# Optimization experiments

Hardware: AMD Instinct MI355X
Metric: run time of the kernel (lower is better)

Reference implementation:

```python
import jax, jax.numpy as jnp
import numpy as np

N, E = 50000, 800000
IN_DIM, HID, OUT_DIM = 512, 64, 40


def setup_inputs() -> dict:
    key = jax.random.key(0)
    ks = jax.random.split(key, 7)
    X = jax.random.normal(ks[0], (N, IN_DIM), dtype=jnp.float32)
    edges = jax.random.randint(ks[1], (2, E), 0, N, dtype=jnp.int64)
    # GCNConv weight (glorot) and bias
    W1 = jax.random.normal(ks[2], (IN_DIM, HID), dtype=jnp.float32) / np.sqrt(IN_DIM)
    b1 = jnp.zeros((HID,), dtype=jnp.float32)
    # fc Linear
    Wfc = jax.random.normal(ks[3], (OUT_DIM, HID), dtype=jnp.float32) / np.sqrt(HID)
    bfc = jax.random.normal(ks[4], (OUT_DIM,), dtype=jnp.float32) * 0.01
    return {"X": X, "edges": edges, "W1": W1, "b1": b1, "Wfc": Wfc, "bfc": bfc}


def gcn_conv(x, src, dst, W, b, n):
    # PyG GCNConv: transform, add self-loops, symmetric D^-1/2 A D^-1/2 norm,
    # scatter-add messages at destination, add bias.
    h = x @ W  # [N, HID]
    loop = jnp.arange(n, dtype=src.dtype)
    src = jnp.concatenate([src, loop])
    dst = jnp.concatenate([dst, loop])
    deg = jax.ops.segment_sum(jnp.ones_like(dst, dtype=h.dtype), dst, num_segments=n)
    dinv = jnp.where(deg > 0, jax.lax.rsqrt(deg), 0.0)
    coef = dinv[src] * dinv[dst]  # [E+N]
    msgs = coef[:, None] * h[src]  # gather + scale
    agg = jax.ops.segment_sum(msgs, dst, num_segments=n)  # scatter-add
    return agg + b


def reference(X, edges, W1, b1, Wfc, bfc):
    n = X.shape[0]
    src, dst = edges[0], edges[1]
    h = jax.nn.relu(gcn_conv(X, src, dst, W1, b1, n))  # [N, HID]
    return h @ Wfc.T + bfc  # [N, OUT_DIM]
```

## Files before the change

kernel.cpp:

```cpp
#include <hip/hip_runtime.h>
#include <hip/hip_bf16.h>

typedef unsigned short u16;
typedef __bf16 bf16_8 __attribute__((ext_vector_type(8)));
typedef float f32_4 __attribute__((ext_vector_type(4)));

#define IN_DIM 512
#define HID 64
#define OUT_DIM 40
#define CAP 64
#define CF_BLOCKS 512

__global__ void k_prep(const float* __restrict__ W1, u16* __restrict__ W1t,
                       int* __restrict__ cnt, int n) {
    int i = blockIdx.x * 256 + threadIdx.x;
    if (i < n) cnt[i] = 0;
    if (i < IN_DIM * HID) {
        int k = i / HID, o = i % HID;
        __hip_bfloat16 v = __float2bfloat16(W1[i]);
        W1t[o * IN_DIM + k] = *reinterpret_cast<u16*>(&v);
    }
}

__launch_bounds__(256)
__global__ void k_work(const float* __restrict__ X, const u16* __restrict__ W1t,
                       const int* __restrict__ src, const int* __restrict__ dst,
                       int* cnt, u16* __restrict__ csr, u16* __restrict__ hs,
                       int N, int E, int NT) {
    __shared__ __align__(16) u16 As[2][64 * 40];
    const int t = threadIdx.x;

    if ((int)blockIdx.x >= NT) {
        const int slice = (int)blockIdx.x & 7;
        const int rank  = ((int)blockIdx.x - NT) >> 3;
        const int lo = (int)(((long)slice * N) >> 3);
        const int hi = (int)(((long)(slice + 1) * N) >> 3);
        const int stride = 64 * 256;
        int e = rank * 256 + t;
        for (; e + 3 * stride < E; e += 4 * stride) {
            int d0 = dst[e];
            int d1 = dst[e + stride];
            int d2 = dst[e + 2 * stride];
            int d3 = dst[e + 3 * stride];
            if (d0 >= lo && d0 < hi) {
                int p = atomicAdd(&cnt[d0], 1);
                if (p < CAP) csr[(size_t)d0 * CAP + p] = (u16)src[e];
            }
            if (d1 >= lo && d1 < hi) {
                int p = atomicAdd(&cnt[d1], 1);
                if (p < CAP) csr[(size_t)d1 * CAP + p] = (u16)src[e + stride];
            }
            if (d2 >= lo && d2 < hi) {
                int p = atomicAdd(&cnt[d2], 1);
                if (p < CAP) csr[(size_t)d2 * CAP + p] = (u16)src[e + 2 * stride];
            }
            if (d3 >= lo && d3 < hi) {
                int p = atomicAdd(&cnt[d3], 1);
                if (p < CAP) csr[(size_t)d3 * CAP + p] = (u16)src[e + 3 * stride];
            }
        }
        for (; e < E; e += stride) {
            int d = dst[e];
            if (d >= lo && d < hi) {
                int p = atomicAdd(&cnt[d], 1);
                if (p < CAP) csr[(size_t)d * CAP + p] = (u16)src[e];
            }
        }
        return;
    }

    const int wave = t >> 6;
    const int lane = t & 63;
    const int m = lane & 15;
    const int quad = lane >> 4;
    const int n0 = blockIdx.x * 64;

    f32_4 acc[4];
    #pragma unroll
    for (int c = 0; c < 4; c++) acc[c] = (f32_4){0.f, 0.f, 0.f, 0.f};

    const int r_st = t >> 2;
    const int k_st = (t & 3) * 8;

    int row = n0 + r_st; if (row >= N) row = N - 1;
    const float* xp = X + (size_t)row * IN_DIM + k_st;

    f32_4 x0 = *reinterpret_cast<const f32_4*>(xp);
    f32_4 x1 = *reinterpret_cast<const f32_4*>(xp + 4);

    int buf = 0;
    for (int k0 = 0; k0 < IN_DIM; k0 += 32) {
        u16 xb[8];
        #pragma unroll
        for (int q = 0; q < 4; q++) {
            __hip_bfloat16 c0 = __float2bfloat16(x0[q]);
            __hip_bfloat16 c1 = __float2bfloat16(x1[q]);
            xb[q]     = *reinterpret_cast<u16*>(&c0);
            xb[4 + q] = *reinterpret_cast<u16*>(&c1);
        }
        *reinterpret_cast<uint4*>(&As[buf][r_st * 40 + k_st]) = *reinterpret_cast<uint4*>(xb);
        __syncthreads();

        if (k0 + 32 < IN_DIM) {
            x0 = *reinterpret_cast<const f32_4*>(xp + k0 + 32);
            x1 = *reinterpret_cast<const f32_4*>(xp + k0 + 36);
        }

        bf16_8 a = *reinterpret_cast<const bf16_8*>(&As[buf][(wave * 16 + m) * 40 + quad * 8]);
        #pragma unroll
        for (int c = 0; c < 4; c++) {
            bf16_8 b = *reinterpret_cast<const bf16_8*>(
                W1t + (size_t)(c * 16 + m) * IN_DIM + k0 + quad * 8);
            acc[c] = __builtin_amdgcn_mfma_f32_16x16x32_bf16(a, b, acc[c], 0, 0, 0);
        }
        buf ^= 1;
    }

    const int nbase = n0 + wave * 16 + quad * 4;
    #pragma unroll
    for (int r = 0; r < 4; r++) {
        int n = nbase + r;
        if (n < N) {
            #pragma unroll
            for (int c = 0; c < 4; c++) {
                __hip_bfloat16 hv = __float2bfloat16(acc[c][r]);
                hs[(size_t)n * HID + c * 16 + m] = *reinterpret_cast<u16*>(&hv);
            }
        }
    }
}

__global__ void k_scale(u16* __restrict__ hs, const int* __restrict__ cnt, int N) {
    int i = blockIdx.x * 256 + threadIdx.x;
    int node = i >> 3;
    if (node >= N) return;
    float dv = rsqrtf((float)cnt[node] + 1.0f);
    uint4 v = *reinterpret_cast<uint4*>(hs + (size_t)i * 8);
    uint vv[4] = {v.x, v.y, v.z, v.w};
    u16 o[8];
    #pragma unroll
    for (int q = 0; q < 4; q++) {
        float lo = __uint_as_float(vv[q] << 16) * dv;
        float hi = __uint_as_float(vv[q] & 0xFFFF0000u) * dv;
        __hip_bfloat16 bl_ = __float2bfloat16(lo);
        __hip_bfloat16 bh_ = __float2bfloat16(hi);
        o[2 * q]     = *reinterpret_cast<u16*>(&bl_);
        o[2 * q + 1] = *reinterpret_cast<u16*>(&bh_);
    }
    *reinterpret_cast<uint4*>(hs + (size_t)i * 8) = *reinterpret_cast<uint4*>(o);
}

__device__ __forceinline__ void acc_add(f32_4& a, uint2 v) {
    a[0] += __uint_as_float(v.x << 16);
    a[1] += __uint_as_float(v.x & 0xFFFF0000u);
    a[2] += __uint_as_float(v.y << 16);
    a[3] += __uint_as_float(v.y & 0xFFFF0000u);
}

#define SHP 72

__launch_bounds__(256)
__global__ void k_aggfc(const u16* __restrict__ hs, const u16* __restrict__ csr,
                        const int* __restrict__ cnt, const float* __restrict__ b1,
                        const float* __restrict__ Wfc, const float* __restrict__ bfc,
                        float* __restrict__ out, int N) {
    __shared__ __align__(16) u16 shb[16 * SHP];
    __shared__ __align__(16) u16 wfb[48 * SHP];
    __shared__ float bl[48];
    const int t = threadIdx.x;

    for (int i = t; i < 48 * HID; i += 256) {
        int o = i / HID, k = i % HID;
        float v = (o < OUT_DIM) ? Wfc[o * HID + k] : 0.f;
        __hip_bfloat16 b = __float2bfloat16(v);
        wfb[o * SHP + k] = *reinterpret_cast<u16*>(&b);
    }
    if (t < 48) bl[t] = (t < OUT_DIM) ? bfc[t] : 0.f;

    const int g = t >> 4, l = t & 15;
    const int n = blockIdx.x * 16 + g;

    if (n < N) {
        const uint2* hs2 = reinterpret_cast<const uint2*>(hs);
        f32_4 aa[4];
        #pragma unroll
        for (int q = 0; q < 4; q++) aa[q] = (f32_4){0.f, 0.f, 0.f, 0.f};
        const float dvn = rsqrtf((float)cnt[n] + 1.0f);
        acc_add(aa[0], hs2[(size_t)n * 16 + l]);
        int deg = cnt[n]; if (deg > CAP) deg = CAP;
        uint2 cv = reinterpret_cast<const uint2*>(csr + (size_t)n * CAP)[l];
        const int nn1 = N - 1;
        for (int j = 0; j < deg; j += 16) {
            int base = j >> 2;
            uint wx[4], wy[4];
            #pragma unroll
            for (int q = 0; q < 4; q++) {
                wx[q] = __shfl(cv.x, base + q, 16);
                wy[q] = __shfl(cv.y, base + q, 16);
            }
            int s[16];
            #pragma unroll
            for (int q = 0; q < 4; q++) {
                s[4 * q + 0] = (int)(wx[q] & 0xffff);
                s[4 * q + 1] = (int)(wx[q] >> 16);
                s[4 * q + 2] = (int)(wy[q] & 0xffff);
                s[4 * q + 3] = (int)(wy[q] >> 16);
            }
            uint2 v[16];
            #pragma unroll
            for (int i = 0; i < 16; i++) {
                int si = s[i] < nn1 ? s[i] : nn1;
                v[i] = hs2[(size_t)si * 16 + l];
            }
            #pragma unroll
            for (int i = 0; i < 16; i++) {
                if (j + i >= deg) { v[i].x = 0u; v[i].y = 0u; }
                acc_add(aa[i & 3], v[i]);
            }
        }
        f32_4 acc = (aa[0] + aa[1]) + (aa[2] + aa[3]);
        u16 rb[4];
        #pragma unroll
        for (int q = 0; q < 4; q++) {
            float x = dvn * acc[q] + b1[l * 4 + q];
            x = x > 0.f ? x : 0.f;
            __hip_bfloat16 hb = __float2bfloat16(x);
            rb[q] = *reinterpret_cast<u16*>(&hb);
        }
        *reinterpret_cast<uint2*>(&shb[g * SHP + l * 4]) = *reinterpret_cast<uint2*>(rb);
    }
    __syncthreads();

    const int wave = t >> 6;
    const int lane = t & 63;
    const int m = lane & 15;
    const int quad = lane >> 4;
    if (wave < 3) {
        bf16_8 a0 = *reinterpret_cast<const bf16_8*>(&shb[m * SHP + quad * 8]);
        bf16_8 a1 = *reinterpret_cast<const bf16_8*>(&shb[m * SHP + 32 + quad * 8]);
        bf16_8 b0 = *reinterpret_cast<const bf16_8*>(&wfb[(wave * 16 + m) * SHP + quad * 8]);
        bf16_8 b1 = *reinterpret_cast<const bf16_8*>(&wfb[(wave * 16 + m) * SHP + 32 + quad * 8]);
        f32_4 c = (f32_4){0.f, 0.f, 0.f, 0.f};
        c = __builtin_amdgcn_mfma_f32_16x16x32_bf16(a0, b0, c, 0, 0, 0);
        c = __builtin_amdgcn_mfma_f32_16x16x32_bf16(a1, b1, c, 0, 0, 0);
        const int o = wave * 16 + m;
        if (o < OUT_DIM) {
            const int base = blockIdx.x * 16;
            #pragma unroll
            for (int r = 0; r < 4; r++) {
                int node = base + quad * 4 + r;
                if (node < N) out[(size_t)node * OUT_DIM + o] = c[r] + bl[o];
            }
        }
    }
}


extern "C" void kernel_launch(void* const* d_in, const int* in_sizes, int n_in,
                              void* d_out, int out_size, void* d_ws, size_t ws_size,
                              hipStream_t stream) {
    const float* X   = (const float*)d_in[0];
    const int* edges = (const int*)d_in[1];
    const float* W1  = (const float*)d_in[2];
    const float* b1  = (const float*)d_in[3];
    const float* Wfc = (const float*)d_in[4];
    const float* bfc = (const float*)d_in[5];

    const int N = in_sizes[0] / IN_DIM;
    const int E = in_sizes[1] / 2;
    const int* src = edges;
    const int* dst = edges + E;

    char* p = (char*)d_ws;
    auto carve = [&](size_t bytes) -> char* {
        char* r = p;
        p += (bytes + 255) & ~(size_t)255;
        return r;
    };
    u16* W1t = (u16*)carve((size_t)IN_DIM * HID * 2);
    u16* hs  = (u16*)carve((size_t)N * HID * 2);
    int* cnt = (int*)carve((size_t)N * 4);
    u16* csr = (u16*)carve((size_t)N * CAP * 2);

    const int nb = (N + 255) / 256;
    const int NT = (N + 63) / 64;

    k_prep <<<nb, 256, 0, stream>>>(W1, W1t, cnt, N);
    k_work <<<NT + CF_BLOCKS, 256, 0, stream>>>(X, W1t, src, dst, cnt, csr, hs, N, E, NT);
    k_scale<<<(N * 8 + 255) / 256, 256, 0, stream>>>(hs, cnt, N);
    k_aggfc<<<(N + 15) / 16, 256, 0, stream>>>(hs, csr, cnt, b1, Wfc, bfc,
                                               (float*)d_out, N);
}
```

Measured before the change: 249.4 us.

## Widen GEMM K-step to 64 and simplify CSR fill to unpartitioned atomics

The GEMM part of k_work now handles 64 K-elements per iteration, with a wider padded LDS tile, two MFMAs per output column block and an extra barrier per iteration. This halves the number of loop iterations and barriers and raises in-flight global loads per thread. Separately, the CSR-building blocks no longer split destinations into 8 slices with a 4-way unrolled scan. Each edge is now processed once with a grid-stride loop, which removes the redundant dst reads across slices but loses the locality of atomics grouped by slice.

```diff
diff --git a/kernel.cpp b/kernel.cpp
--- a/kernel.cpp
+++ b/kernel.cpp
@@ -27,44 +27,16 @@
                        const int* __restrict__ src, const int* __restrict__ dst,
                        int* cnt, u16* __restrict__ csr, u16* __restrict__ hs,
                        int N, int E, int NT) {
-    __shared__ __align__(16) u16 As[2][64 * 40];
+    __shared__ __align__(16) u16 As[2][64 * 72];
     const int t = threadIdx.x;
 
     if ((int)blockIdx.x >= NT) {
-        const int slice = (int)blockIdx.x & 7;
-        const int rank  = ((int)blockIdx.x - NT) >> 3;
-        const int lo = (int)(((long)slice * N) >> 3);
-        const int hi = (int)(((long)(slice + 1) * N) >> 3);
-        const int stride = 64 * 256;
-        int e = rank * 256 + t;
-        for (; e + 3 * stride < E; e += 4 * stride) {
-            int d0 = dst[e];
-            int d1 = dst[e + stride];
-            int d2 = dst[e + 2 * stride];
-            int d3 = dst[e + 3 * stride];
-            if (d0 >= lo && d0 < hi) {
-                int p = atomicAdd(&cnt[d0], 1);
-                if (p < CAP) csr[(size_t)d0 * CAP + p] = (u16)src[e];
-            }
-            if (d1 >= lo && d1 < hi) {
-                int p = atomicAdd(&cnt[d1], 1);
-                if (p < CAP) csr[(size_t)d1 * CAP + p] = (u16)src[e + stride];
-            }
-            if (d2 >= lo && d2 < hi) {
-                int p = atomicAdd(&cnt[d2], 1);
-                if (p < CAP) csr[(size_t)d2 * CAP + p] = (u16)src[e + 2 * stride];
-            }
-            if (d3 >= lo && d3 < hi) {
-                int p = atomicAdd(&cnt[d3], 1);
-                if (p < CAP) csr[(size_t)d3 * CAP + p] = (u16)src[e + 3 * stride];
-            }
-        }
-        for (; e < E; e += stride) {
+        int tid = ((int)blockIdx.x - NT) * 256 + t;
+        int stride = CF_BLOCKS * 256;
+        for (int e = tid; e < E; e += stride) {
             int d = dst[e];
-            if (d >= lo && d < hi) {
-                int p = atomicAdd(&cnt[d], 1);
-                if (p < CAP) csr[(size_t)d * CAP + p] = (u16)src[e];
-            }
+            int p = atomicAdd(&cnt[d], 1);
+            if (p < CAP) csr[(size_t)d * CAP + p] = (u16)src[e];
         }
         return;
     }
@@ -80,39 +52,54 @@
     for (int c = 0; c < 4; c++) acc[c] = (f32_4){0.f, 0.f, 0.f, 0.f};
 
     const int r_st = t >> 2;
-    const int k_st = (t & 3) * 8;
+    const int c2 = t & 3;
 
     int row = n0 + r_st; if (row >= N) row = N - 1;
-    const float* xp = X + (size_t)row * IN_DIM + k_st;
+    const float* xp = X + (size_t)row * IN_DIM + c2 * 16;
 
     f32_4 x0 = *reinterpret_cast<const f32_4*>(xp);
     f32_4 x1 = *reinterpret_cast<const f32_4*>(xp + 4);
+    f32_4 x2 = *reinterpret_cast<const f32_4*>(xp + 8);
+    f32_4 x3 = *reinterpret_cast<const f32_4*>(xp + 12);
 
     int buf = 0;
-    for (int k0 = 0; k0 < IN_DIM; k0 += 32) {
-        u16 xb[8];
+    for (int k0 = 0; k0 < IN_DIM; k0 += 64) {
+        u16 xb[16];
         #pragma unroll
         for (int q = 0; q < 4; q++) {
             __hip_bfloat16 c0 = __float2bfloat16(x0[q]);
             __hip_bfloat16 c1 = __float2bfloat16(x1[q]);
-            xb[q]     = *reinterpret_cast<u16*>(&c0);
-            xb[4 + q] = *reinterpret_cast<u16*>(&c1);
-        }
-        *reinterpret_cast<uint4*>(&As[buf][r_st * 40 + k_st]) = *reinterpret_cast<uint4*>(xb);
+            __hip_bfloat16 c2_ = __float2bfloat16(x2[q]);
+            __hip_bfloat16 c3 = __float2bfloat16(x3[q]);
+            xb[q]      = *reinterpret_cast<u16*>(&c0);
+            xb[4 + q]  = *reinterpret_cast<u16*>(&c1);
+            xb[8 + q]  = *reinterpret_cast<u16*>(&c2_);
+            xb[12 + q] = *reinterpret_cast<u16*>(&c3);
+        }
+        u16* wp = &As[buf][r_st * 72 + c2 * 16];
+        *reinterpret_cast<uint4*>(wp)     = *reinterpret_cast<uint4*>(&xb[0]);
+        *reinterpret_cast<uint4*>(wp + 8) = *reinterpret_cast<uint4*>(&xb[8]);
         __syncthreads();
 
-        if (k0 + 32 < IN_DIM) {
-            x0 = *reinterpret_cast<const f32_4*>(xp + k0 + 32);
-            x1 = *reinterpret_cast<const f32_4*>(xp + k0 + 36);
-        }
-
-        bf16_8 a = *reinterpret_cast<const bf16_8*>(&As[buf][(wave * 16 + m) * 40 + quad * 8]);
+        if (k0 + 64 < IN_DIM) {
+            x0 = *reinterpret_cast<const f32_4*>(xp + k0 + 64);
+            x1 = *reinterpret_cast<const f32_4*>(xp + k0 + 68);
+            x2 = *reinterpret_cast<const f32_4*>(xp + k0 + 72);
+            x3 = *reinterpret_cast<const f32_4*>(xp + k0 + 76);
+        }
+
+        bf16_8 a0 = *reinterpret_cast<const bf16_8*>(&As[buf][(wave * 16 + m) * 72 + quad * 8]);
+        bf16_8 a1 = *reinterpret_cast<const bf16_8*>(&As[buf][(wave * 16 + m) * 72 + 32 + quad * 8]);
         #pragma unroll
         for (int c = 0; c < 4; c++) {
-            bf16_8 b = *reinterpret_cast<const bf16_8*>(
+            bf16_8 b0 = *reinterpret_cast<const bf16_8*>(
                 W1t + (size_t)(c * 16 + m) * IN_DIM + k0 + quad * 8);
-            acc[c] = __builtin_amdgcn_mfma_f32_16x16x32_bf16(a, b, acc[c], 0, 0, 0);
-        }
+            bf16_8 b1 = *reinterpret_cast<const bf16_8*>(
+                W1t + (size_t)(c * 16 + m) * IN_DIM + k0 + 32 + quad * 8);
+            acc[c] = __builtin_amdgcn_mfma_f32_16x16x32_bf16(a0, b0, acc[c], 0, 0, 0);
+            acc[c] = __builtin_amdgcn_mfma_f32_16x16x32_bf16(a1, b1, acc[c], 0, 0, 0);
+        }
+        __syncthreads();
         buf ^= 1;
     }
 
```

After: 233.3 us. 6.5% less time.

## Pre-bucket edges by destination slice before CSR build

Applied to the files above, without the earlier changes.

Adds a bucketing kernel that makes one pass over src/dst, packs each edge into a 32-bit entry (local dst offset, src) and writes it into per-slice, per-segment buckets using wave-ballot aggregated atomics. The CSR-building blocks in k_work then read only their own slice's bucket instead of each of the 8 slices rescanning all edges. This removes the 8x redundant read of the edge arrays at the cost of an extra kernel launch and an intermediate buffer. Entries beyond the fixed bucket capacity are silently dropped, and the packing assumes a slice spans fewer than 65536 nodes.

```diff
diff --git a/kernel.cpp b/kernel.cpp
--- a/kernel.cpp
+++ b/kernel.cpp
@@ -2,6 +2,7 @@
 #include <hip/hip_bf16.h>
 
 typedef unsigned short u16;
+typedef unsigned int u32;
 typedef __bf16 bf16_8 __attribute__((ext_vector_type(8)));
 typedef float f32_4 __attribute__((ext_vector_type(4)));
 
@@ -10,11 +11,15 @@
 #define OUT_DIM 40
 #define CAP 64
 #define CF_BLOCKS 512
+#define NSLICE 8
+#define NSEG 16
+#define SCAP 7168
 
 __global__ void k_prep(const float* __restrict__ W1, u16* __restrict__ W1t,
-                       int* __restrict__ cnt, int n) {
+                       int* __restrict__ cnt, int* __restrict__ tails, int n) {
     int i = blockIdx.x * 256 + threadIdx.x;
     if (i < n) cnt[i] = 0;
+    if (i < NSLICE * NSEG) tails[i] = 0;
     if (i < IN_DIM * HID) {
         int k = i / HID, o = i % HID;
         __hip_bfloat16 v = __float2bfloat16(W1[i]);
@@ -23,8 +28,47 @@
 }
 
 __launch_bounds__(256)
+__global__ void k_bucket(const int* __restrict__ src, const int* __restrict__ dst,
+                         u32* __restrict__ bkt, int* __restrict__ tails, int N, int E) {
+    const int t = threadIdx.x;
+    const int lane = t & 63;
+    const unsigned long long mask_lt = (lane == 0) ? 0ull : ((~0ull) >> (64 - lane));
+    const int seg = (int)blockIdx.x & (NSEG - 1);
+    const int stride = 256 * 256;
+    for (int e = (int)blockIdx.x * 256 + t; ; e += stride) {
+        bool valid = e < E;
+        if (!__any(valid)) break;
+        int d = 0, s = 0, b = 0;
+        u32 entry = 0;
+        if (valid) {
+            d = dst[e];
+            s = src[e];
+            b = (int)((u32)(d * 8) / (u32)N);
+            int lo_b = (b * N + 7) >> 3;
+            entry = ((u32)(d - lo_b) << 16) | (u32)s;
+        }
+        #pragma unroll
+        for (int bb = 0; bb < NSLICE; bb++) {
+            unsigned long long m = __ballot(valid && (b == bb));
+            if (!m) continue;
+            int cnt_m = __popcll(m);
+            int leader = __ffsll((unsigned long long)m) - 1;
+            int base = 0;
+            if (lane == leader) base = atomicAdd(&tails[bb * NSEG + seg], cnt_m);
+            base = __shfl(base, leader);
+            if (valid && b == bb) {
+                int rank = __popcll(m & mask_lt);
+                int idx = base + rank;
+                if (idx < SCAP)
+                    bkt[(size_t)(bb * NSEG + seg) * SCAP + idx] = entry;
+            }
+        }
+    }
+}
+
+__launch_bounds__(256)
 __global__ void k_work(const float* __restrict__ X, const u16* __restrict__ W1t,
-                       const int* __restrict__ src, const int* __restrict__ dst,
+                       const u32* __restrict__ bkt, const int* __restrict__ tails,
                        int* cnt, u16* __restrict__ csr, u16* __restrict__ hs,
                        int N, int E, int NT) {
     __shared__ __align__(16) u16 As[2][64 * 40];
@@ -33,37 +77,17 @@
     if ((int)blockIdx.x >= NT) {
         const int slice = (int)blockIdx.x & 7;
         const int rank  = ((int)blockIdx.x - NT) >> 3;
-        const int lo = (int)(((long)slice * N) >> 3);
-        const int hi = (int)(((long)(slice + 1) * N) >> 3);
-        const int stride = 64 * 256;
-        int e = rank * 256 + t;
-        for (; e + 3 * stride < E; e += 4 * stride) {
-            int d0 = dst[e];
-            int d1 = dst[e + stride];
-            int d2 = dst[e + 2 * stride];
-            int d3 = dst[e + 3 * stride];
-            if (d0 >= lo && d0 < hi) {
-                int p = atomicAdd(&cnt[d0], 1);
-                if (p < CAP) csr[(size_t)d0 * CAP + p] = (u16)src[e];
-            }
-            if (d1 >= lo && d1 < hi) {
-                int p = atomicAdd(&cnt[d1], 1);
-                if (p < CAP) csr[(size_t)d1 * CAP + p] = (u16)src[e + stride];
-            }
-            if (d2 >= lo && d2 < hi) {
-                int p = atomicAdd(&cnt[d2], 1);
-                if (p < CAP) csr[(size_t)d2 * CAP + p] = (u16)src[e + 2 * stride];
-            }
-            if (d3 >= lo && d3 < hi) {
-                int p = atomicAdd(&cnt[d3], 1);
-                if (p < CAP) csr[(size_t)d3 * CAP + p] = (u16)src[e + 3 * stride];
-            }
-        }
-        for (; e < E; e += stride) {
-            int d = dst[e];
-            if (d >= lo && d < hi) {
+        const int lo_b  = (slice * N + 7) >> 3;
+        #pragma unroll 1
+        for (int sg = 0; sg < NSEG; sg++) {
+            int ce = tails[slice * NSEG + sg];
+            if (ce > SCAP) ce = SCAP;
+            const u32* bp = bkt + (size_t)(slice * NSEG + sg) * SCAP;
+            for (int i = rank * 256 + t; i < ce; i += 64 * 256) {
+                u32 en = bp[i];
+                int d = lo_b + (int)(en >> 16);
                 int p = atomicAdd(&cnt[d], 1);
-                if (p < CAP) csr[(size_t)d * CAP + p] = (u16)src[e];
+                if (p < CAP) csr[(size_t)d * CAP + p] = (u16)(en & 0xffffu);
             }
         }
         return;
@@ -277,17 +301,20 @@
         p += (bytes + 255) & ~(size_t)255;
         return r;
     };
-    u16* W1t = (u16*)carve((size_t)IN_DIM * HID * 2);
-    u16* hs  = (u16*)carve((size_t)N * HID * 2);
-    int* cnt = (int*)carve((size_t)N * 4);
-    u16* csr = (u16*)carve((size_t)N * CAP * 2);
+    u16* W1t   = (u16*)carve((size_t)IN_DIM * HID * 2);
+    u16* hs    = (u16*)carve((size_t)N * HID * 2);
+    int* cnt   = (int*)carve((size_t)N * 4);
+    u16* csr   = (u16*)carve((size_t)N * CAP * 2);
+    int* tails = (int*)carve((size_t)NSLICE * NSEG * 4);
+    u32* bkt   = (u32*)carve((size_t)NSLICE * NSEG * SCAP * 4);
 
     const int nb = (N + 255) / 256;
     const int NT = (N + 63) / 64;
 
-    k_prep <<<nb, 256, 0, stream>>>(W1, W1t, cnt, N);
-    k_work <<<NT + CF_BLOCKS, 256, 0, stream>>>(X, W1t, src, dst, cnt, csr, hs, N, E, NT);
-    k_scale<<<(N * 8 + 255) / 256, 256, 0, stream>>>(hs, cnt, N);
-    k_aggfc<<<(N + 15) / 16, 256, 0, stream>>>(hs, csr, cnt, b1, Wfc, bfc,
-                                               (float*)d_out, N);
-}
+    k_prep  <<<nb, 256, 0, stream>>>(W1, W1t, cnt, tails, N);
+    k_bucket<<<256, 256, 0, stream>>>(src, dst, bkt, tails, N, E);
+    k_work  <<<NT + CF_BLOCKS, 256, 0, stream>>>(X, W1t, bkt, tails, cnt, csr, hs, N, E, NT);
+    k_scale <<<(N * 8 + 255) / 256, 256, 0, stream>>>(hs, cnt, N);
+    k_aggfc <<<(N + 15) / 16, 256, 0, stream>>>(hs, csr, cnt, b1, Wfc, bfc,
+                                                (float*)d_out, N);
+}
```

Result: slower. 498.8 us (+100.0%).

## Split fused CSR-build/GEMM kernel and add split-K GEMM with 512 threads

Applied to the files above, without the earlier changes.

Separates the CSR-fill path from the X@W1 GEMM into two kernels launched back to back on the same stream, dropping the 8-way destination-slice filtering in favour of a simple grid-stride edge loop. The GEMM now uses 512-thread blocks that split K=512 into two halves, with the second half's partial sums reduced through shared memory before writing bf16 output. The aim is more memory-level parallelism for the bandwidth-bound X read and a simpler, faster atomic edge scatter. In exchange it loses the overlap of the scatter with the GEMM and adds a shared-memory reduction plus extra shared memory per block.

```diff
diff --git a/kernel.cpp b/kernel.cpp
--- a/kernel.cpp
+++ b/kernel.cpp
@@ -9,7 +9,7 @@
 #define HID 64
 #define OUT_DIM 40
 #define CAP 64
-#define CF_BLOCKS 512
+#define CF_GRID 2048
 
 __global__ void k_prep(const float* __restrict__ W1, u16* __restrict__ W1t,
                        int* __restrict__ cnt, int n) {
@@ -23,53 +23,25 @@
 }
 
 __launch_bounds__(256)
-__global__ void k_work(const float* __restrict__ X, const u16* __restrict__ W1t,
-                       const int* __restrict__ src, const int* __restrict__ dst,
-                       int* cnt, u16* __restrict__ csr, u16* __restrict__ hs,
-                       int N, int E, int NT) {
-    __shared__ __align__(16) u16 As[2][64 * 40];
+__global__ void k_cf(const int* __restrict__ src, const int* __restrict__ dst,
+                     int* cnt, u16* __restrict__ csr, int E) {
+    int e = blockIdx.x * 256 + threadIdx.x;
+    const int stride = CF_GRID * 256;
+    for (; e < E; e += stride) {
+        int d = dst[e];
+        int p = atomicAdd(&cnt[d], 1);
+        if (p < CAP) csr[(size_t)d * CAP + p] = (u16)src[e];
+    }
+}
+
+__launch_bounds__(512)
+__global__ void k_gemm(const float* __restrict__ X, const u16* __restrict__ W1t,
+                       u16* __restrict__ hs, int N) {
+    __shared__ __align__(16) u16 As[2][2][64 * 40];
+    __shared__ __align__(16) float Red[64 * 64];
     const int t = threadIdx.x;
-
-    if ((int)blockIdx.x >= NT) {
-        const int slice = (int)blockIdx.x & 7;
-        const int rank  = ((int)blockIdx.x - NT) >> 3;
-        const int lo = (int)(((long)slice * N) >> 3);
-        const int hi = (int)(((long)(slice + 1) * N) >> 3);
-        const int stride = 64 * 256;
-        int e = rank * 256 + t;
-        for (; e + 3 * stride < E; e += 4 * stride) {
-            int d0 = dst[e];
-            int d1 = dst[e + stride];
-            int d2 = dst[e + 2 * stride];
-            int d3 = dst[e + 3 * stride];
-            if (d0 >= lo && d0 < hi) {
-                int p = atomicAdd(&cnt[d0], 1);
-                if (p < CAP) csr[(size_t)d0 * CAP + p] = (u16)src[e];
-            }
-            if (d1 >= lo && d1 < hi) {
-                int p = atomicAdd(&cnt[d1], 1);
-                if (p < CAP) csr[(size_t)d1 * CAP + p] = (u16)src[e + stride];
-            }
-            if (d2 >= lo && d2 < hi) {
-                int p = atomicAdd(&cnt[d2], 1);
-                if (p < CAP) csr[(size_t)d2 * CAP + p] = (u16)src[e + 2 * stride];
-            }
-            if (d3 >= lo && d3 < hi) {
-                int p = atomicAdd(&cnt[d3], 1);
-                if (p < CAP) csr[(size_t)d3 * CAP + p] = (u16)src[e + 3 * stride];
-            }
-        }
-        for (; e < E; e += stride) {
-            int d = dst[e];
-            if (d >= lo && d < hi) {
-                int p = atomicAdd(&cnt[d], 1);
-                if (p < CAP) csr[(size_t)d * CAP + p] = (u16)src[e];
-            }
-        }
-        return;
-    }
-
-    const int wave = t >> 6;
+    const int g = t >> 8;
+    const int wl = (t >> 6) & 3;
     const int lane = t & 63;
     const int m = lane & 15;
     const int quad = lane >> 4;
@@ -79,17 +51,18 @@
     #pragma unroll
     for (int c = 0; c < 4; c++) acc[c] = (f32_4){0.f, 0.f, 0.f, 0.f};
 
-    const int r_st = t >> 2;
-    const int k_st = (t & 3) * 8;
+    const int tg = t & 255;
+    const int r_st = tg >> 2;
+    const int k_st = (tg & 3) * 8;
 
     int row = n0 + r_st; if (row >= N) row = N - 1;
-    const float* xp = X + (size_t)row * IN_DIM + k_st;
+    const float* xp = X + (size_t)row * IN_DIM + g * 256 + k_st;
 
     f32_4 x0 = *reinterpret_cast<const f32_4*>(xp);
     f32_4 x1 = *reinterpret_cast<const f32_4*>(xp + 4);
 
     int buf = 0;
-    for (int k0 = 0; k0 < IN_DIM; k0 += 32) {
+    for (int ks = 0; ks < 256; ks += 32) {
         u16 xb[8];
         #pragma unroll
         for (int q = 0; q < 4; q++) {
@@ -98,33 +71,44 @@
             xb[q]     = *reinterpret_cast<u16*>(&c0);
             xb[4 + q] = *reinterpret_cast<u16*>(&c1);
         }
-        *reinterpret_cast<uint4*>(&As[buf][r_st * 40 + k_st]) = *reinterpret_cast<uint4*>(xb);
+        *reinterpret_cast<uint4*>(&As[g][buf][r_st * 40 + k_st]) = *reinterpret_cast<uint4*>(xb);
         __syncthreads();
 
-        if (k0 + 32 < IN_DIM) {
-            x0 = *reinterpret_cast<const f32_4*>(xp + k0 + 32);
-            x1 = *reinterpret_cast<const f32_4*>(xp + k0 + 36);
-        }
-
-        bf16_8 a = *reinterpret_cast<const bf16_8*>(&As[buf][(wave * 16 + m) * 40 + quad * 8]);
+        if (ks + 32 < 256) {
+            x0 = *reinterpret_cast<const f32_4*>(xp + ks + 32);
+            x1 = *reinterpret_cast<const f32_4*>(xp + ks + 36);
+        }
+
+        bf16_8 a = *reinterpret_cast<const bf16_8*>(&As[g][buf][(wl * 16 + m) * 40 + quad * 8]);
         #pragma unroll
         for (int c = 0; c < 4; c++) {
             bf16_8 b = *reinterpret_cast<const bf16_8*>(
-                W1t + (size_t)(c * 16 + m) * IN_DIM + k0 + quad * 8);
+                W1t + (size_t)(c * 16 + m) * IN_DIM + g * 256 + ks + quad * 8);
             acc[c] = __builtin_amdgcn_mfma_f32_16x16x32_bf16(a, b, acc[c], 0, 0, 0);
         }
         buf ^= 1;
     }
 
-    const int nbase = n0 + wave * 16 + quad * 4;
-    #pragma unroll
-    for (int r = 0; r < 4; r++) {
-        int n = nbase + r;
-        if (n < N) {
-            #pragma unroll
-            for (int c = 0; c < 4; c++) {
-                __hip_bfloat16 hv = __float2bfloat16(acc[c][r]);
-                hs[(size_t)n * HID + c * 16 + m] = *reinterpret_cast<u16*>(&hv);
+    if (g == 1) {
+        #pragma unroll
+        for (int r = 0; r < 4; r++)
+            #pragma unroll
+            for (int c = 0; c < 4; c++)
+                Red[(wl * 16 + quad * 4 + r) * 64 + c * 16 + m] = acc[c][r];
+    }
+    __syncthreads();
+    if (g == 0) {
+        const int nbase = n0 + wl * 16 + quad * 4;
+        #pragma unroll
+        for (int r = 0; r < 4; r++) {
+            int n = nbase + r;
+            if (n < N) {
+                #pragma unroll
+                for (int c = 0; c < 4; c++) {
+                    float s = acc[c][r] + Red[(wl * 16 + quad * 4 + r) * 64 + c * 16 + m];
+                    __hip_bfloat16 hv = __float2bfloat16(s);
+                    hs[(size_t)n * HID + c * 16 + m] = *reinterpret_cast<u16*>(&hv);
+                }
             }
         }
     }
@@ -286,7 +270,8 @@
     const int NT = (N + 63) / 64;
 
     k_prep <<<nb, 256, 0, stream>>>(W1, W1t, cnt, N);
-    k_work <<<NT + CF_BLOCKS, 256, 0, stream>>>(X, W1t, src, dst, cnt, csr, hs, N, E, NT);
+    k_cf   <<<CF_GRID, 256, 0, stream>>>(src, dst, cnt, csr, E);
+    k_gemm <<<NT, 512, 0, stream>>>(X, W1t, hs, N);
     k_scale<<<(N * 8 + 255) / 256, 256, 0, stream>>>(hs, cnt, N);
     k_aggfc<<<(N + 15) / 16, 256, 0, stream>>>(hs, csr, cnt, b1, Wfc, bfc,
                                                (float*)d_out, N);
```

New measurement: 259.2 us. 3.9% more time.
